# Kernel optimization log

Measured on AMD Instinct MI355X. Metric: run time of the kernel, lower is better.

The kernel has to match this reference:

```python
import jax, jax.numpy as jnp
import numpy as np

T = 4096
EMBED = 1024
HEADS = 16


def setup_inputs() -> dict:
    key = jax.random.key(0)
    kx, kq, kk, kv = jax.random.split(key, 4)
    bound = 1.0 / np.sqrt(EMBED)
    x = jax.random.normal(kx, (T, EMBED), dtype=jnp.float32)
    Wq = jax.random.uniform(kq, (EMBED, EMBED), minval=-bound, maxval=bound, dtype=jnp.float32)
    Wk = jax.random.uniform(kk, (EMBED, EMBED), minval=-bound, maxval=bound, dtype=jnp.float32)
    Wv = jax.random.uniform(kv, (EMBED, EMBED), minval=-bound, maxval=bound, dtype=jnp.float32)
    return {"x": x, "Wq": Wq, "Wk": Wk, "Wv": Wv}


def reference(x, Wq, Wk, Wv):
    t, e = x.shape
    h = HEADS
    c = e // h  # head dim
    q = (x @ Wq).reshape(t, h, c)
    k = (x @ Wk).reshape(t, h, c)
    v = (x @ Wv).reshape(t, h, c)
    # scores: [h, t, t]
    scores = jnp.einsum('qhc,khc->hqk', q, k) / jnp.sqrt(jnp.asarray(c, x.dtype))
    causal = jnp.tril(jnp.ones((t, t), dtype=bool))
    scores = jnp.where(causal[None, :, :], scores, -jnp.inf)  # same as + log(tril)
    p = jax.nn.softmax(scores, axis=-1)
    y = jnp.einsum('hqk,khc->qhc', p, v)  # [t, h, c]
    return y.reshape(t, e)
```

## Files before the change

### kernel.cpp

```cpp
#include <hip/hip_runtime.h>
#include <hip/hip_bf16.h>

#define T_SEQ 4096
#define EMB 1024
#define NH 16
#define HD 64
#define QBLK 128
#define KVB 64
#define DEFER_THR 10.0f

typedef float f32x4 __attribute__((ext_vector_type(4)));
typedef float f32x16 __attribute__((ext_vector_type(16)));
typedef short short8 __attribute__((ext_vector_type(8)));
typedef short short4v __attribute__((ext_vector_type(4)));

__device__ inline unsigned short f2bf(float f) {
  union { float f; unsigned u; } a; a.f = f;
  unsigned r = a.u + 0x7fffu + ((a.u >> 16) & 1u);
  return (unsigned short)(r >> 16);
}
#if __has_builtin(__builtin_amdgcn_exp2f)
#define EXP2F(x) __builtin_amdgcn_exp2f(x)
#else
#define EXP2F(x) exp2f(x)
#endif
#define GLL16(g, l) __builtin_amdgcn_global_load_lds( \
    (const __attribute__((address_space(1))) void*)(g), \
    (__attribute__((address_space(3))) void*)(l), 16, 0, 0)

__global__ __launch_bounds__(256) void cast_x_kernel(const float* __restrict__ in,
                                                     unsigned short* __restrict__ out) {
  int i = (blockIdx.x * 256 + threadIdx.x) * 8;
  float4 a = *(const float4*)(in + i);
  float4 b = *(const float4*)(in + i + 4);
  uint4 o;
  o.x = f2bf(a.x) | ((unsigned)f2bf(a.y) << 16);
  o.y = f2bf(a.z) | ((unsigned)f2bf(a.w) << 16);
  o.z = f2bf(b.x) | ((unsigned)f2bf(b.y) << 16);
  o.w = f2bf(b.z) | ((unsigned)f2bf(b.w) << 16);
  *(uint4*)(out + i) = o;
}

__global__ __launch_bounds__(256) void transpose_cast_kernel(const float* __restrict__ Wq,
                                                             const float* __restrict__ Wk,
                                                             const float* __restrict__ Wv,
                                                             unsigned short* __restrict__ WTall) {
  int z = blockIdx.z;
  const float* W = (z == 0) ? Wq : ((z == 1) ? Wk : Wv);
  unsigned short* WT = WTall + (size_t)z * EMB * EMB;
  __shared__ unsigned short tile[32][33];
  int tx = threadIdx.x & 31, ty = threadIdx.x >> 5;
  int bn = blockIdx.x * 32, bk = blockIdx.y * 32;
#pragma unroll
  for (int p = 0; p < 4; p++)
    tile[ty + p * 8][tx] = f2bf(W[(size_t)(bk + ty + p * 8) * EMB + bn + tx]);
  __syncthreads();
#pragma unroll
  for (int p = 0; p < 4; p++)
    WT[(size_t)(bn + ty + p * 8) * EMB + bk + tx] = tile[tx][ty + p * 8];
}

__global__ __launch_bounds__(256) void transpose_v_kernel(const unsigned short* __restrict__ V,
                                                          unsigned short* __restrict__ VT) {
  int h = blockIdx.z;
  int t0 = blockIdx.x * 32, d0 = blockIdx.y * 32;
  __shared__ unsigned short tl[32][33];
  int tx = threadIdx.x & 31, ty = threadIdx.x >> 5;
#pragma unroll
  for (int p = 0; p < 4; p++)
    tl[ty + p * 8][tx] = V[(size_t)(t0 + ty + p * 8) * EMB + h * HD + d0 + tx];
  __syncthreads();
#pragma unroll
  for (int p = 0; p < 4; p++)
    VT[(size_t)(h * HD + d0 + ty + p * 8) * T_SEQ + t0 + tx] = tl[tx][ty + p * 8];
}

__global__ __launch_bounds__(256) void gemm_qkv(const unsigned short* __restrict__ Xb,
                                                const unsigned short* __restrict__ WTall,
                                                unsigned short* __restrict__ QKV) {
  int z = blockIdx.z;
  const unsigned short* Bt = WTall + (size_t)z * EMB * EMB;
  unsigned short* Out = QKV + (size_t)z * T_SEQ * EMB;

  __shared__ __align__(16) unsigned short sA[128 * 32];
  __shared__ __align__(16) unsigned short sB[128 * 32];

  int m0 = blockIdx.x * 128, n0 = blockIdx.y * 128;
  int tid = threadIdx.x;
  int lane = tid & 63, wid = tid >> 6;
  int wr = wid >> 1, wc = wid & 1;
  int fr = lane & 15, fq = lane >> 4;

  int r0 = tid >> 2, o0 = (tid & 3) * 8;
  int r1 = (tid + 256) >> 2;

  f32x4 acc[4][4] = {};

  for (int k0 = 0; k0 < EMB; k0 += 32) {
    __syncthreads();
    GLL16(Xb + (size_t)(m0 + r0) * EMB + k0 + o0, sA + (size_t)tid * 8);
    GLL16(Xb + (size_t)(m0 + r1) * EMB + k0 + o0, sA + (size_t)(tid + 256) * 8);
    GLL16(Bt + (size_t)(n0 + r0) * EMB + k0 + o0, sB + (size_t)tid * 8);
    GLL16(Bt + (size_t)(n0 + r1) * EMB + k0 + o0, sB + (size_t)(tid + 256) * 8);
    asm volatile("s_waitcnt vmcnt(0)" ::: "memory");
    __syncthreads();

    short8 aF[4], bF[4];
#pragma unroll
    for (int i = 0; i < 4; i++) {
      aF[i] = *(const short8*)(sA + (wr * 64 + i * 16 + fr) * 32 + fq * 8);
      bF[i] = *(const short8*)(sB + (wc * 64 + i * 16 + fr) * 32 + fq * 8);
    }
#pragma unroll
    for (int i = 0; i < 4; i++)
#pragma unroll
      for (int j = 0; j < 4; j++)
        acc[i][j] = __builtin_amdgcn_mfma_f32_16x16x32_bf16(aF[i], bF[j], acc[i][j], 0, 0, 0);
  }

  float scale = (z == 0) ? 0.1803368801111204f : 1.0f;
#pragma unroll
  for (int i = 0; i < 4; i++)
#pragma unroll
    for (int j = 0; j < 4; j++)
#pragma unroll
      for (int r = 0; r < 4; r++) {
        int row = m0 + wr * 64 + i * 16 + fq * 4 + r;
        int col = n0 + wc * 64 + j * 16 + fr;
        Out[(size_t)row * EMB + col] = f2bf(acc[i][j][r] * scale);
      }
}

__global__ __launch_bounds__(256) void attn_kernel(const unsigned short* __restrict__ Qb,
                                                   const unsigned short* __restrict__ Kb,
                                                   const unsigned short* __restrict__ VTg,
                                                   float* __restrict__ Opart,
                                                   float* __restrict__ Mst,
                                                   float* __restrict__ Lst) {
  int c = (gridDim.x - 1) - blockIdx.x;
  int h = blockIdx.y;
  int z = blockIdx.z;
  int q0 = c * QBLK;
  int tid = threadIdx.x;
  int lane = tid & 63, w = tid >> 6;
  int ql = lane & 31, hi = lane >> 5;

  __shared__ __align__(16) unsigned short smem[14336];
  unsigned short* sK = smem;
  unsigned short* sVT = smem + 64 * 72;
  unsigned short* sP = smem + 2 * 64 * 72 + w * (32 * 40);

  int wq0 = q0 + w * 32;
  int qg = wq0 + ql;

  short8 qf[4];
#pragma unroll
  for (int ks = 0; ks < 4; ks++)
    qf[ks] = *(const short8*)(Qb + (size_t)qg * EMB + h * HD + ks * 16 + hi * 8);

  f32x16 oT0 = {}, oT1 = {};
  float m = -1e30f, lsum = 0.f;

  int sr = tid >> 3;
  int scs = (tid & 7) * 8;

  int wqmax = wq0 + 31;
  int ntot = 2 * c + 2;

  {
    int kv0 = z * KVB;
    short8 ka = *(const short8*)(Kb + (size_t)(kv0 + sr) * EMB + h * HD + scs);
    short8 kb = *(const short8*)(Kb + (size_t)(kv0 + sr + 32) * EMB + h * HD + scs);
    short8 va = *(const short8*)(VTg + (size_t)(h * HD + sr) * T_SEQ + kv0 + scs);
    short8 vb = *(const short8*)(VTg + (size_t)(h * HD + sr + 32) * T_SEQ + kv0 + scs);

    for (int t = z; t < ntot; t += 2) {
      int kv0c = t * KVB;
      __syncthreads();
      *(short8*)(sK + sr * 72 + scs) = ka;
      *(short8*)(sK + (sr + 32) * 72 + scs) = kb;
      *(short8*)(sVT + sr * 72 + scs) = va;
      *(short8*)(sVT + (sr + 32) * 72 + scs) = vb;
      __syncthreads();

      if (t + 2 < ntot) {
        int kv1 = kv0c + 2 * KVB;
        ka = *(const short8*)(Kb + (size_t)(kv1 + sr) * EMB + h * HD + scs);
        kb = *(const short8*)(Kb + (size_t)(kv1 + sr + 32) * EMB + h * HD + scs);
        va = *(const short8*)(VTg + (size_t)(h * HD + sr) * T_SEQ + kv1 + scs);
        vb = *(const short8*)(VTg + (size_t)(h * HD + sr + 32) * T_SEQ + kv1 + scs);
      }

#pragma unroll
      for (int s = 0; s < 2; s++) {
        int kvs = kv0c + s * 32;
        if (kvs <= wqmax) {
          f32x16 st = {};
          __builtin_amdgcn_s_setprio(1);
#pragma unroll
          for (int ks = 0; ks < 4; ks++) {
            short8 kf = *(const short8*)(sK + (s * 32 + ql) * 72 + ks * 16 + hi * 8);
            st = __builtin_amdgcn_mfma_f32_32x32x16_bf16(kf, qf[ks], st, 0, 0, 0);
          }
          __builtin_amdgcn_s_setprio(0);
          if (kvs + 31 > wq0) {
#pragma unroll
            for (int r = 0; r < 16; r++) {
              int kvg = kvs + (r & 3) + 8 * (r >> 2) + 4 * hi;
              if (kvg > qg) st[r] = -1e30f;
            }
          }
          float a0 = fmaxf(fmaxf(st[0], st[1]), st[2]);
          float a1 = fmaxf(fmaxf(st[3], st[4]), st[5]);
          float a2 = fmaxf(fmaxf(st[6], st[7]), st[8]);
          float a3 = fmaxf(fmaxf(st[9], st[10]), st[11]);
          float a4 = fmaxf(fmaxf(st[12], st[13]), st[14]);
          float mt = fmaxf(fmaxf(fmaxf(a0, a1), a2), fmaxf(fmaxf(a3, a4), st[15]));
          mt = fmaxf(mt, __shfl_xor(mt, 32));
          if (!__all(mt - m <= DEFER_THR)) {
            float mnew = fmaxf(m, mt);
            float al = EXP2F(m - mnew);
            lsum *= al;
#pragma unroll
            for (int r = 0; r < 16; r++) { oT0[r] *= al; oT1[r] *= al; }
            m = mnew;
          }
#pragma unroll
          for (int r = 0; r < 16; r++) st[r] = EXP2F(st[r] - m);
          float s0 = (st[0] + st[1]) + (st[2] + st[3]);
          float s1 = (st[4] + st[5]) + (st[6] + st[7]);
          float s2 = (st[8] + st[9]) + (st[10] + st[11]);
          float s3 = (st[12] + st[13]) + (st[14] + st[15]);
          float ls = (s0 + s1) + (s2 + s3);
          ls += __shfl_xor(ls, 32);
          lsum += ls;

#pragma unroll
          for (int g = 0; g < 4; g++) {
            __hip_bfloat162 plo = __float22bfloat162_rn(float2{st[g * 4 + 0], st[g * 4 + 1]});
            __hip_bfloat162 phi = __float22bfloat162_rn(float2{st[g * 4 + 2], st[g * 4 + 3]});
            union { __hip_bfloat162 hh[2]; short4v s4; } u4;
            u4.hh[0] = plo; u4.hh[1] = phi;
            *(short4v*)(sP + ql * 40 + g * 8 + hi * 4) = u4.s4;
          }
          asm volatile("s_waitcnt lgkmcnt(0)" ::: "memory");
          __builtin_amdgcn_sched_barrier(0);

          __builtin_amdgcn_s_setprio(1);
#pragma unroll
          for (int ksp = 0; ksp < 2; ksp++) {
            short8 pa = *(const short8*)(sP + ql * 40 + ksp * 16 + hi * 8);
            int cb = s * 32 + ksp * 16 + hi * 8;
            short8 v0 = *(const short8*)(sVT + (0 * 32 + ql) * 72 + cb);
            short8 v1 = *(const short8*)(sVT + (1 * 32 + ql) * 72 + cb);
            oT0 = __builtin_amdgcn_mfma_f32_32x32x16_bf16(v0, pa, oT0, 0, 0, 0);
            oT1 = __builtin_amdgcn_mfma_f32_32x32x16_bf16(v1, pa, oT1, 0, 0, 0);
          }
          __builtin_amdgcn_s_setprio(0);
        }
      }
    }
  }

  if (hi == 0) {
    Mst[((size_t)z * NH + h) * T_SEQ + qg] = m;
    Lst[((size_t)z * NH + h) * T_SEQ + qg] = lsum;
  }

  float* Od = Opart + (size_t)z * T_SEQ * EMB;
  float* sw = (float*)smem + w * (32 * 36);
  int orow = lane >> 1, ocol = (lane & 1) * 16;
#pragma unroll
  for (int dt = 0; dt < 2; dt++) {
    __syncthreads();
#pragma unroll
    for (int r = 0; r < 16; r++) {
      int dl = (r & 3) + 8 * (r >> 2) + 4 * hi;
      sw[ql * 36 + dl] = dt ? oT1[r] : oT0[r];
    }
    __syncthreads();
#pragma unroll
    for (int cc = 0; cc < 4; cc++) {
      f32x4 vv = *(const f32x4*)(sw + orow * 36 + ocol + cc * 4);
      *(f32x4*)(Od + (size_t)(wq0 + orow) * EMB + h * HD + dt * 32 + ocol + cc * 4) = vv;
    }
  }
}

__global__ __launch_bounds__(256) void combine_kernel(const float* __restrict__ Opart,
                                                      const float* __restrict__ Mst,
                                                      const float* __restrict__ Lst,
                                                      float* __restrict__ out) {
  int i = (blockIdx.x * 256 + threadIdx.x) * 8;
  int t = i >> 10, e = i & (EMB - 1), h = e >> 6;
  float m0 = Mst[(size_t)h * T_SEQ + t], m1 = Mst[(size_t)(NH + h) * T_SEQ + t];
  float l0 = Lst[(size_t)h * T_SEQ + t], l1 = Lst[(size_t)(NH + h) * T_SEQ + t];
  float mF = fmaxf(m0, m1);
  float w0 = EXP2F(m0 - mF), w1 = EXP2F(m1 - mF);
  float inv = 1.0f / (l0 * w0 + l1 * w1);
  w0 *= inv; w1 *= inv;
  const float* O1 = Opart + (size_t)T_SEQ * EMB;
  f32x4 a0 = *(const f32x4*)(Opart + i), a1 = *(const f32x4*)(Opart + i + 4);
  f32x4 b0 = *(const f32x4*)(O1 + i),    b1 = *(const f32x4*)(O1 + i + 4);
  f32x4 r0, r1;
#pragma unroll
  for (int j = 0; j < 4; j++) { r0[j] = a0[j] * w0 + b0[j] * w1; r1[j] = a1[j] * w0 + b1[j] * w1; }
  *(f32x4*)(out + i) = r0;
  *(f32x4*)(out + i + 4) = r1;
}

extern "C" void kernel_launch(void* const* d_in, const int* in_sizes, int n_in,
                              void* d_out, int out_size, void* d_ws, size_t ws_size,
                              hipStream_t stream) {
  const float* x  = (const float*)d_in[0];
  const float* Wq = (const float*)d_in[1];
  const float* Wk = (const float*)d_in[2];
  const float* Wv = (const float*)d_in[3];
  float* out = (float*)d_out;

  unsigned short* Qb = (unsigned short*)d_ws;
  unsigned short* Kb = Qb + (size_t)T_SEQ * EMB;
  unsigned short* Vb = Kb + (size_t)T_SEQ * EMB;
  unsigned short* VT = Vb + (size_t)T_SEQ * EMB;
  unsigned short* Xb = VT + (size_t)T_SEQ * EMB;
  unsigned short* WT = Xb + (size_t)T_SEQ * EMB;
  float* Opart = (float*)(WT + (size_t)3 * EMB * EMB);
  float* Mst = Opart + (size_t)2 * T_SEQ * EMB;
  float* Lst = Mst + (size_t)2 * NH * T_SEQ;

  cast_x_kernel<<<(T_SEQ * EMB) / (256 * 8), 256, 0, stream>>>(x, Xb);
  dim3 tg(EMB / 32, EMB / 32, 3);
  transpose_cast_kernel<<<tg, 256, 0, stream>>>(Wq, Wk, Wv, WT);
  dim3 gg(T_SEQ / 128, EMB / 128, 3);
  gemm_qkv<<<gg, 256, 0, stream>>>(Xb, WT, Qb);
  dim3 tv(T_SEQ / 32, HD / 32, NH);
  transpose_v_kernel<<<tv, 256, 0, stream>>>(Vb, VT);
  dim3 ag(T_SEQ / QBLK, NH, 2);
  attn_kernel<<<ag, 256, 0, stream>>>(Qb, Kb, VT, Opart, Mst, Lst);
  combine_kernel<<<(T_SEQ * EMB) / (256 * 8), 256, 0, stream>>>(Opart, Mst, Lst, out);
}
```

Measured before the change: 245.4 us.

## Pair causal query blocks per workgroup and split KV four ways

Each attention workgroup now handles two query blocks, p and 31-p, so causal work per workgroup is roughly equal instead of triangular. The KV range is split into four interleaved partitions instead of two, keeping the same number of workgroups while shortening each one's serial KV loop. The combine kernel merges four partial outputs using their max and sum statistics. This costs twice as much partial-output memory and more read traffic in the combine step, and the workspace must be large enough to hold four partial buffers.

```diff
diff --git a/kernel.cpp b/kernel.cpp
--- a/kernel.cpp
+++ b/kernel.cpp
@@ -7,6 +7,7 @@
 #define HD 64
 #define QBLK 128
 #define KVB 64
+#define ZS 4
 #define DEFER_THR 10.0f
 
 typedef float f32x4 __attribute__((ext_vector_type(4)));
@@ -137,10 +138,9 @@
                                                    float* __restrict__ Opart,
                                                    float* __restrict__ Mst,
                                                    float* __restrict__ Lst) {
-  int c = (gridDim.x - 1) - blockIdx.x;
+  int p = blockIdx.x;
   int h = blockIdx.y;
   int z = blockIdx.z;
-  int q0 = c * QBLK;
   int tid = threadIdx.x;
   int lane = tid & 63, w = tid >> 6;
   int ql = lane & 31, hi = lane >> 5;
@@ -150,31 +150,33 @@
   unsigned short* sVT = smem + 64 * 72;
   unsigned short* sP = smem + 2 * 64 * 72 + w * (32 * 40);
 
-  int wq0 = q0 + w * 32;
-  int qg = wq0 + ql;
-
-  short8 qf[4];
-#pragma unroll
-  for (int ks = 0; ks < 4; ks++)
-    qf[ks] = *(const short8*)(Qb + (size_t)qg * EMB + h * HD + ks * 16 + hi * 8);
-
-  f32x16 oT0 = {}, oT1 = {};
-  float m = -1e30f, lsum = 0.f;
-
   int sr = tid >> 3;
   int scs = (tid & 7) * 8;
 
-  int wqmax = wq0 + 31;
-  int ntot = 2 * c + 2;
-
-  {
-    int kv0 = z * KVB;
-    short8 ka = *(const short8*)(Kb + (size_t)(kv0 + sr) * EMB + h * HD + scs);
-    short8 kb = *(const short8*)(Kb + (size_t)(kv0 + sr + 32) * EMB + h * HD + scs);
-    short8 va = *(const short8*)(VTg + (size_t)(h * HD + sr) * T_SEQ + kv0 + scs);
-    short8 vb = *(const short8*)(VTg + (size_t)(h * HD + sr + 32) * T_SEQ + kv0 + scs);
-
-    for (int t = z; t < ntot; t += 2) {
+#pragma unroll 1
+  for (int side = 0; side < 2; side++) {
+    int c = side ? (31 - p) : p;
+    int q0 = c * QBLK;
+    int wq0 = q0 + w * 32;
+    int qg = wq0 + ql;
+    int wqmax = wq0 + 31;
+    int ntot = 2 * c + 2;
+
+    short8 qf[4];
+#pragma unroll
+    for (int ks = 0; ks < 4; ks++)
+      qf[ks] = *(const short8*)(Qb + (size_t)qg * EMB + h * HD + ks * 16 + hi * 8);
+
+    f32x16 oT0 = {}, oT1 = {};
+    float m = -1e30f, lsum = 0.f;
+
+    int kvp = z * KVB;
+    short8 ka = *(const short8*)(Kb + (size_t)(kvp + sr) * EMB + h * HD + scs);
+    short8 kb = *(const short8*)(Kb + (size_t)(kvp + sr + 32) * EMB + h * HD + scs);
+    short8 va = *(const short8*)(VTg + (size_t)(h * HD + sr) * T_SEQ + kvp + scs);
+    short8 vb = *(const short8*)(VTg + (size_t)(h * HD + sr + 32) * T_SEQ + kvp + scs);
+
+    for (int t = z; t < ntot; t += ZS) {
       int kv0c = t * KVB;
       __syncthreads();
       *(short8*)(sK + sr * 72 + scs) = ka;
@@ -183,8 +185,8 @@
       *(short8*)(sVT + (sr + 32) * 72 + scs) = vb;
       __syncthreads();
 
-      if (t + 2 < ntot) {
-        int kv1 = kv0c + 2 * KVB;
+      if (t + ZS < ntot) {
+        int kv1 = kv0c + ZS * KVB;
         ka = *(const short8*)(Kb + (size_t)(kv1 + sr) * EMB + h * HD + scs);
         kb = *(const short8*)(Kb + (size_t)(kv1 + sr + 32) * EMB + h * HD + scs);
         va = *(const short8*)(VTg + (size_t)(h * HD + sr) * T_SEQ + kv1 + scs);
@@ -260,29 +262,29 @@
         }
       }
     }
-  }
-
-  if (hi == 0) {
-    Mst[((size_t)z * NH + h) * T_SEQ + qg] = m;
-    Lst[((size_t)z * NH + h) * T_SEQ + qg] = lsum;
-  }
-
-  float* Od = Opart + (size_t)z * T_SEQ * EMB;
-  float* sw = (float*)smem + w * (32 * 36);
-  int orow = lane >> 1, ocol = (lane & 1) * 16;
-#pragma unroll
-  for (int dt = 0; dt < 2; dt++) {
-    __syncthreads();
-#pragma unroll
-    for (int r = 0; r < 16; r++) {
-      int dl = (r & 3) + 8 * (r >> 2) + 4 * hi;
-      sw[ql * 36 + dl] = dt ? oT1[r] : oT0[r];
+
+    if (hi == 0) {
+      Mst[((size_t)z * NH + h) * T_SEQ + qg] = m;
+      Lst[((size_t)z * NH + h) * T_SEQ + qg] = lsum;
     }
-    __syncthreads();
-#pragma unroll
-    for (int cc = 0; cc < 4; cc++) {
-      f32x4 vv = *(const f32x4*)(sw + orow * 36 + ocol + cc * 4);
-      *(f32x4*)(Od + (size_t)(wq0 + orow) * EMB + h * HD + dt * 32 + ocol + cc * 4) = vv;
+
+    float* Od = Opart + (size_t)z * T_SEQ * EMB;
+    float* sw = (float*)smem + w * (32 * 36);
+    int orow = lane >> 1, ocol = (lane & 1) * 16;
+#pragma unroll
+    for (int dt = 0; dt < 2; dt++) {
+      __syncthreads();
+#pragma unroll
+      for (int r = 0; r < 16; r++) {
+        int dl = (r & 3) + 8 * (r >> 2) + 4 * hi;
+        sw[ql * 36 + dl] = dt ? oT1[r] : oT0[r];
+      }
+      __syncthreads();
+#pragma unroll
+      for (int cc = 0; cc < 4; cc++) {
+        f32x4 vv = *(const f32x4*)(sw + orow * 36 + ocol + cc * 4);
+        *(f32x4*)(Od + (size_t)(wq0 + orow) * EMB + h * HD + dt * 32 + ocol + cc * 4) = vv;
+      }
     }
   }
 }
@@ -293,18 +295,26 @@
                                                       float* __restrict__ out) {
   int i = (blockIdx.x * 256 + threadIdx.x) * 8;
   int t = i >> 10, e = i & (EMB - 1), h = e >> 6;
-  float m0 = Mst[(size_t)h * T_SEQ + t], m1 = Mst[(size_t)(NH + h) * T_SEQ + t];
-  float l0 = Lst[(size_t)h * T_SEQ + t], l1 = Lst[(size_t)(NH + h) * T_SEQ + t];
-  float mF = fmaxf(m0, m1);
-  float w0 = EXP2F(m0 - mF), w1 = EXP2F(m1 - mF);
-  float inv = 1.0f / (l0 * w0 + l1 * w1);
-  w0 *= inv; w1 *= inv;
-  const float* O1 = Opart + (size_t)T_SEQ * EMB;
-  f32x4 a0 = *(const f32x4*)(Opart + i), a1 = *(const f32x4*)(Opart + i + 4);
-  f32x4 b0 = *(const f32x4*)(O1 + i),    b1 = *(const f32x4*)(O1 + i + 4);
-  f32x4 r0, r1;
-#pragma unroll
-  for (int j = 0; j < 4; j++) { r0[j] = a0[j] * w0 + b0[j] * w1; r1[j] = a1[j] * w0 + b1[j] * w1; }
+  float mz[ZS], lz[ZS];
+#pragma unroll
+  for (int z = 0; z < ZS; z++) {
+    mz[z] = Mst[((size_t)z * NH + h) * T_SEQ + t];
+    lz[z] = Lst[((size_t)z * NH + h) * T_SEQ + t];
+  }
+  float mF = fmaxf(fmaxf(mz[0], mz[1]), fmaxf(mz[2], mz[3]));
+  float wz[ZS], denom = 0.f;
+#pragma unroll
+  for (int z = 0; z < ZS; z++) { wz[z] = EXP2F(mz[z] - mF); denom += lz[z] * wz[z]; }
+  float inv = 1.0f / denom;
+  f32x4 r0 = {}, r1 = {};
+#pragma unroll
+  for (int z = 0; z < ZS; z++) {
+    const float* Oz = Opart + (size_t)z * T_SEQ * EMB;
+    f32x4 a0 = *(const f32x4*)(Oz + i), a1 = *(const f32x4*)(Oz + i + 4);
+    float wgt = wz[z] * inv;
+#pragma unroll
+    for (int j = 0; j < 4; j++) { r0[j] += a0[j] * wgt; r1[j] += a1[j] * wgt; }
+  }
   *(f32x4*)(out + i) = r0;
   *(f32x4*)(out + i + 4) = r1;
 }
@@ -325,8 +335,8 @@
   unsigned short* Xb = VT + (size_t)T_SEQ * EMB;
   unsigned short* WT = Xb + (size_t)T_SEQ * EMB;
   float* Opart = (float*)(WT + (size_t)3 * EMB * EMB);
-  float* Mst = Opart + (size_t)2 * T_SEQ * EMB;
-  float* Lst = Mst + (size_t)2 * NH * T_SEQ;
+  float* Mst = Opart + (size_t)ZS * T_SEQ * EMB;
+  float* Lst = Mst + (size_t)ZS * NH * T_SEQ;
 
   cast_x_kernel<<<(T_SEQ * EMB) / (256 * 8), 256, 0, stream>>>(x, Xb);
   dim3 tg(EMB / 32, EMB / 32, 3);
@@ -335,7 +345,7 @@
   gemm_qkv<<<gg, 256, 0, stream>>>(Xb, WT, Qb);
   dim3 tv(T_SEQ / 32, HD / 32, NH);
   transpose_v_kernel<<<tv, 256, 0, stream>>>(Vb, VT);
-  dim3 ag(T_SEQ / QBLK, NH, 2);
+  dim3 ag(T_SEQ / QBLK / 2, NH, ZS);
   attn_kernel<<<ag, 256, 0, stream>>>(Qb, Kb, VT, Opart, Mst, Lst);
   combine_kernel<<<(T_SEQ * EMB) / (256 * 8), 256, 0, stream>>>(Opart, Mst, Lst, out);
 }
```

After: 213.2 us. 1.15x faster.
